# Optimization experiments

Measured on AMD Instinct MI355X. Metric: run time of the kernel, lower is better.

Reference implementation:

```python
import jax, jax.numpy as jnp
import numpy as np

N_ENT, N_REL, E, S, W, C = 1000000, 1000, 128, 8, 64, 1024


def setup_inputs() -> dict:
    key = jax.random.key(0)
    ks = jax.random.split(key, 12)
    sc = 0.02
    return {
        "ent_emb": jax.random.normal(ks[0], (N_ENT, E), jnp.float32),
        "rel_emb": jax.random.normal(ks[1], (N_REL, E), jnp.float32),
        "relation": jax.random.normal(ks[2], (E,), jnp.float32),
        "W1": jax.random.normal(ks[3], (3 * E, 3 * E), jnp.float32) * sc,
        "b1": jnp.zeros((3 * E,), jnp.float32),
        "W2": jax.random.normal(ks[4], (3 * E, 2 * E), jnp.float32) * sc,
        "b2": jnp.zeros((2 * E,), jnp.float32),
        "lstm_k": jax.random.normal(ks[5], (2 * E, 4 * E), jnp.float32) * sc,
        "lstm_r": jax.random.normal(ks[6], (E, 4 * E), jnp.float32) * sc,
        "lstm_b": jnp.zeros((4 * E,), jnp.float32),
        "cand_rel_ids": jax.random.randint(ks[7], (S, W, C), 0, N_REL),
        "cand_ent_ids": jax.random.randint(ks[8], (S, W, C), 0, N_ENT),
        "start_ent": jax.random.randint(ks[9], (W,), 0, N_ENT),
    }


def reference(ent_emb, rel_emb, relation, W1, b1, W2, b2, lstm_k, lstm_r, lstm_b,
              cand_rel_ids, cand_ent_ids, start_ent):
    # Batched, fixed-shape version of LSTMFinder.paths_between's hot loop:
    # per step: posterior MLP -> candidate gather+dot -> softmax -> global top-k
    # over (beam, candidate) -> LSTMCell state update for selected beams.
    rel_b = jnp.broadcast_to(relation, (W, E))

    def step(carry, xs):
        h, c, hist, cur = carry              # h,c,hist: [W,E]; cur: [W] int
        cr, ce = xs                          # [W,C] candidate rel/ent ids
        # posterior_mlp(concat(ent_enb, history_vector, relation))
        feat_in = jnp.concatenate([ent_emb[cur], hist, rel_b], axis=-1)   # [W,3E]
        hmid = jax.nn.relu(feat_in @ W1 + b1)
        feature = jax.nn.relu(hmid @ W2 + b2)                              # [W,2E]
        # candidate embeddings concat(rel_vec, ent_vec)
        cand_emb = jnp.concatenate([rel_emb[cr], ent_emb[ce]], axis=-1)    # [W,C,2E]
        scores = jnp.einsum('wcd,wd->wc', cand_emb, feature)               # [W,C]
        probs = jax.nn.softmax(scores, axis=-1)                            # per-path softmax
        # top_n_of_2d_choices over the full (beam, candidate) grid
        _, idx = jax.lax.top_k(probs.reshape(-1), W)
        parent = idx // C
        sel = idx % C
        inp = cand_emb[parent, sel]                                        # [W,2E]
        hp, cp = h[parent], c[parent]
        # keras LSTMCell: z = x@K + h@R + b, gates order i,f,g,o
        z = inp @ lstm_k + hp @ lstm_r + lstm_b
        i, f, g, o = jnp.split(z, 4, axis=-1)
        c_new = jax.nn.sigmoid(f) * cp + jax.nn.sigmoid(i) * jnp.tanh(g)
        h_new = jax.nn.sigmoid(o) * jnp.tanh(c_new)
        cur_new = ce[parent, sel]
        return (h_new, c_new, h_new, cur_new), probs

    z0 = jnp.zeros((W, E), jnp.float32)
    carry0 = (z0, z0, z0, start_ent)
    _, probs_all = jax.lax.scan(step, carry0, (cand_rel_ids, cand_ent_ids))
    return probs_all   # [S, W, C]
```

## Files before the change

kernel.cpp:

```cpp
#include <hip/hip_runtime.h>
#include <stdint.h>

#define E 128
#define W 64
#define C 1024
#define S 8
#define NBUCK 4096

typedef unsigned long long u64;
typedef unsigned int u32;

__device__ __forceinline__ float sigm(float x) { return 1.0f / (1.0f + expf(-x)); }

__device__ __forceinline__ int suffix_threshold(u32* hist, u32* wtot, int* s_B,
                                                int t, int lane, int wid) {
  const int b0 = t << 2;
  const u32 v0 = hist[b0], v1 = hist[b0 + 1], v2 = hist[b0 + 2], v3 = hist[b0 + 3];
  const u32 s3 = v3, s2 = v2 + s3, s1 = v1 + s2, s0 = v0 + s1;
  u32 incl = s0;
#pragma unroll
  for (int off = 1; off < 64; off <<= 1) {
    const u32 n = __shfl_down(incl, off, 64);
    if (lane + off < 64) incl += n;
  }
  if (lane == 0) wtot[wid] = incl;
  __syncthreads();
  u32 wsuf = 0;
  for (int i = wid + 1; i < 16; ++i) wsuf += wtot[i];
  const u32 above = wsuf + (incl - s0);
  hist[b0]     = above + s0;
  hist[b0 + 1] = above + s1;
  hist[b0 + 2] = above + s2;
  hist[b0 + 3] = above + s3;
  __syncthreads();
#pragma unroll
  for (int j = 0; j < 4; ++j) {
    const int b = b0 + j;
    const u32 here = hist[b];
    const u32 nxt = (b + 1 < NBUCK) ? hist[b + 1] : 0u;
    if (here >= 64u && nxt < 64u) *s_B = b;
  }
  __syncthreads();
  return *s_B;
}

__global__ __launch_bounds__(1024) void kA(
    int step,
    const float* __restrict__ ent_emb, const float* __restrict__ rel_emb,
    const float* __restrict__ relation,
    const float* __restrict__ W1, const float* __restrict__ b1,
    const float* __restrict__ W2, const float* __restrict__ b2,
    const float* __restrict__ lstm_k, const float* __restrict__ lstm_r,
    const float* __restrict__ lstm_b,
    const int* __restrict__ cand_rel_ids, const int* __restrict__ cand_ent_ids,
    const int* __restrict__ start_ent,
    float* __restrict__ Hst, float* __restrict__ Cst,
    float* __restrict__ rconstb,
    const u64* __restrict__ rowtop,
    float* __restrict__ featb)
{
  const int w = blockIdx.x, t = threadIdx.x;
  const int lane = t & 63, wid = t >> 6;
  __shared__ __align__(16) float xin[384];
  __shared__ __align__(16) float xcat2[256];
  __shared__ __align__(16) float z[512];
  __shared__ __align__(16) float hmid[384];
  __shared__ float sredpad[16];
  __shared__ u32 wtot[16];
  __shared__ int s_par, s_rid, s_eid, s_cnt, s_B;
  __shared__ __align__(16) unsigned char arena[32768];
  u32* hist = (u32*)arena;
  u64* coll = (u64*)arena;
  float4* zacc = (float4*)arena;
  (void)sredpad;

  float* Hn = Hst + (size_t)(step & 1) * W * E;
  float* Cn = Cst + (size_t)(step & 1) * W * E;
  const float* Hp = Hst + (size_t)((step + 1) & 1) * W * E;
  const float* Cp = Cst + (size_t)((step + 1) & 1) * W * E;

  if (step == 0) {
    const int cur = start_ent[w];
    if (t < 128) {
      xcat2[t] = ent_emb[(size_t)cur * E + t];
      xcat2[128 + t] = 0.f;
      Hn[w * E + t] = 0.f;
      Cn[w * E + t] = 0.f;
    }
    if (t < 384) {
      const int jg = t % 96, ks = t / 96;
      const int j0 = jg << 2, k0 = ks << 5;
      float4 acc = make_float4(0.f, 0.f, 0.f, 0.f);
#pragma unroll 8
      for (int kk = 0; kk < 32; ++kk) {
        const int k = k0 + kk;
        const float4 wt = *(const float4*)(W1 + (size_t)(256 + k) * 384 + j0);
        const float xk = relation[k];
        acc.x += xk * wt.x; acc.y += xk * wt.y;
        acc.z += xk * wt.z; acc.w += xk * wt.w;
      }
      zacc[t] = acc;
    }
    __syncthreads();
    if (t < 96) {
      float4 a = zacc[t];
#pragma unroll
      for (int sl = 1; sl < 4; ++sl) {
        const float4 bq = zacc[sl * 96 + t];
        a.x += bq.x; a.y += bq.y; a.z += bq.z; a.w += bq.w;
      }
      ((float4*)z)[t] = a;
      *(float4*)(rconstb + (t << 2)) = a;
    }
    __syncthreads();
  } else {
    if (t == 0) s_cnt = 0;
    ((uint4*)hist)[t] = make_uint4(0u, 0u, 0u, 0u);
    __syncthreads();
    u64 myk[4];
#pragma unroll
    for (int j = 0; j < 4; ++j) {
      myk[j] = rowtop[t + (j << 10)];
      atomicAdd(&hist[(u32)(myk[j] >> 51) & 0xFFFu], 1u);
    }
    __syncthreads();
    const int B = suffix_threshold(hist, wtot, &s_B, t, lane, wid);
#pragma unroll
    for (int j = 0; j < 4; ++j)
      if ((int)((myk[j] >> 51) & 0xFFFull) >= B) coll[atomicAdd(&s_cnt, 1)] = myk[j];
    __syncthreads();
    const int M = s_cnt;
    for (int i = t; i < M; i += 1024) {
      const u64 ki = coll[i];
      int r = 0;
      for (int j = 0; j < M; ++j) r += (coll[j] > ki);
      if (r == w) {
        const u32 flat = ~(u32)(ki & 0xFFFFFFFFull);
        const int p = (int)(flat >> 10);
        const int sl = (int)(flat & 1023u);
        const size_t cbase = (size_t)(step - 1) * W * C + (size_t)p * C + sl;
        s_par = p;
        s_rid = cand_rel_ids[cbase];
        s_eid = cand_ent_ids[cbase];
      }
    }
    __syncthreads();
    const int par = s_par, rid = s_rid, eid = s_eid;
    if (t < 384) {
      float v;
      if (t < 128) v = rel_emb[(size_t)rid * E + t];
      else if (t < 256) v = ent_emb[(size_t)eid * E + (t - 128)];
      else v = Hp[(size_t)par * E + (t - 256)];
      xin[t] = v;
    } else if (t < 512) {
      xcat2[t - 384] = ent_emb[(size_t)eid * E + (t - 384)];
    }
    __syncthreads();
    {
      const int ks = t >> 7, jg = t & 127;
      const int j0 = jg << 2, k0 = ks * 48;
      float4 acc = make_float4(0.f, 0.f, 0.f, 0.f);
#pragma unroll 8
      for (int kk = 0; kk < 48; ++kk) {
        const int k = k0 + kk;
        const float* Wp = (k < 256) ? (lstm_k + (size_t)k * 512 + j0)
                                    : (lstm_r + (size_t)(k - 256) * 512 + j0);
        const float4 wt = *(const float4*)Wp;
        const float xk = xin[k];
        acc.x += xk * wt.x; acc.y += xk * wt.y;
        acc.z += xk * wt.z; acc.w += xk * wt.w;
      }
      zacc[t] = acc;
    }
    __syncthreads();
    if (t < 128) {
      float4 a = zacc[t];
#pragma unroll
      for (int sl = 1; sl < 8; ++sl) {
        const float4 bq = zacc[sl * 128 + t];
        a.x += bq.x; a.y += bq.y; a.z += bq.z; a.w += bq.w;
      }
      const float4 bb = *(const float4*)(lstm_b + (t << 2));
      a.x += bb.x; a.y += bb.y; a.z += bb.z; a.w += bb.w;
      ((float4*)z)[t] = a;
    }
    __syncthreads();
    if (t < 128) {
      const float zi = z[t], zf = z[128 + t], zg = z[256 + t], zo = z[384 + t];
      const float cp = Cp[(size_t)par * E + t];
      const float cn = sigm(zf) * cp + sigm(zi) * tanhf(zg);
      const float hn = sigm(zo) * tanhf(cn);
      xcat2[128 + t] = hn;
      Hn[w * E + t] = hn;
      Cn[w * E + t] = cn;
    }
    __syncthreads();
  }

  if (t < 768) {
    const int jg = t % 96, ks = t / 96;
    const int j0 = jg << 2, k0 = ks << 5;
    float4 acc = make_float4(0.f, 0.f, 0.f, 0.f);
#pragma unroll 8
    for (int kk = 0; kk < 32; ++kk) {
      const int k = k0 + kk;
      const float4 wt = *(const float4*)(W1 + (size_t)k * 384 + j0);
      const float xk = xcat2[k];
      acc.x += xk * wt.x; acc.y += xk * wt.y;
      acc.z += xk * wt.z; acc.w += xk * wt.w;
    }
    zacc[t] = acc;
  }
  __syncthreads();
  if (t < 96) {
    float4 a = zacc[t];
#pragma unroll
    for (int sl = 1; sl < 8; ++sl) {
      const float4 bq = zacc[sl * 96 + t];
      a.x += bq.x; a.y += bq.y; a.z += bq.z; a.w += bq.w;
    }
    const float4 rc = (step == 0) ? ((const float4*)z)[t]
                                  : *(const float4*)(rconstb + (t << 2));
    const float4 bb = *(const float4*)(b1 + (t << 2));
    float4 hv;
    hv.x = fmaxf(a.x + rc.x + bb.x, 0.f);
    hv.y = fmaxf(a.y + rc.y + bb.y, 0.f);
    hv.z = fmaxf(a.z + rc.z + bb.z, 0.f);
    hv.w = fmaxf(a.w + rc.w + bb.w, 0.f);
    ((float4*)hmid)[t] = hv;
  }
  __syncthreads();

  {
    const int jg = t & 63, ks = t >> 6;
    const int j0 = jg << 2, k0 = ks * 24;
    float4 acc = make_float4(0.f, 0.f, 0.f, 0.f);
#pragma unroll 8
    for (int kk = 0; kk < 24; ++kk) {
      const int k = k0 + kk;
      const float4 wt = *(const float4*)(W2 + (size_t)k * 256 + j0);
      const float xk = hmid[k];
      acc.x += xk * wt.x; acc.y += xk * wt.y;
      acc.z += xk * wt.z; acc.w += xk * wt.w;
    }
    zacc[t] = acc;
  }
  __syncthreads();
  if (t < 64) {
    float4 a = zacc[t];
#pragma unroll
    for (int sl = 1; sl < 16; ++sl) {
      const float4 bq = zacc[sl * 64 + t];
      a.x += bq.x; a.y += bq.y; a.z += bq.z; a.w += bq.w;
    }
    const float4 bb = *(const float4*)(b2 + (t << 2));
    float4 fv;
    fv.x = fmaxf(a.x + bb.x, 0.f);
    fv.y = fmaxf(a.y + bb.y, 0.f);
    fv.z = fmaxf(a.z + bb.z, 0.f);
    fv.w = fmaxf(a.w + bb.w, 0.f);
    ((float4*)(featb + (size_t)w * 256))[t] = fv;
  }
}

__global__ __launch_bounds__(512) void kB(
    int step,
    const float* __restrict__ ent_emb, const float* __restrict__ rel_emb,
    const int* __restrict__ cand_rel_ids, const int* __restrict__ cand_ent_ids,
    const float* __restrict__ featb, float* __restrict__ scoresb)
{
  const int b = blockIdx.x, tid = threadIdx.x;
  const int w = b >> 3, c0 = (b & 7) << 7;
  __shared__ __align__(16) float featl[256];
  __shared__ int srid[128], seid[128];

  const size_t idbase = (size_t)step * W * C + (size_t)w * C + c0;
  if (tid < 256) featl[tid] = featb[(size_t)w * 256 + tid];
  else if (tid < 384) srid[tid - 256] = cand_rel_ids[idbase + (tid - 256)];
  else seid[tid - 384] = cand_ent_ids[idbase + (tid - 384)];
  __syncthreads();

  const int cl = tid >> 2, j = tid & 3;
  const float4* rp = (const float4*)(rel_emb + (size_t)srid[cl] * E);
  const float4* ep = (const float4*)(ent_emb + (size_t)seid[cl] * E);
  const float4* f4 = (const float4*)featl;
  float ax = 0.f, ay = 0.f, az = 0.f, aw = 0.f;
#pragma unroll
  for (int i = 0; i < 8; ++i) {
    const float4 r = rp[j + 4 * i], f = f4[j + 4 * i];
    ax += r.x * f.x; ay += r.y * f.y; az += r.z * f.z; aw += r.w * f.w;
  }
#pragma unroll
  for (int i = 0; i < 8; ++i) {
    const float4 e = ep[j + 4 * i], f = f4[32 + j + 4 * i];
    ax += e.x * f.x; ay += e.y * f.y; az += e.z * f.z; aw += e.w * f.w;
  }
  float acc = (ax + ay) + (az + aw);
  acc += __shfl_xor(acc, 1, 64);
  acc += __shfl_xor(acc, 2, 64);
  if (j == 0) scoresb[(size_t)w * C + c0 + cl] = acc;
}

__global__ __launch_bounds__(1024) void kC(
    int step, int last, const float* __restrict__ scoresb,
    float* __restrict__ out, u64* __restrict__ rowtop)
{
  const int w = blockIdx.x, t = threadIdx.x;
  const int lane = t & 63, wid = t >> 6;
  __shared__ float sred[16];
  __shared__ float s_m, s_inv;
  __shared__ u32 wtot[16];
  __shared__ int s_cnt, s_B;
  __shared__ __align__(16) unsigned char arena[32768];
  u32* hist = (u32*)arena;
  u64* coll = (u64*)arena;

  const float score = scoresb[(size_t)w * C + t];

  float v = score;
#pragma unroll
  for (int d = 32; d; d >>= 1) v = fmaxf(v, __shfl_xor(v, d, 64));
  if (lane == 0) sred[wid] = v;
  __syncthreads();
  if (t == 0) {
    float mm = sred[0];
#pragma unroll
    for (int i = 1; i < 16; ++i) mm = fmaxf(mm, sred[i]);
    s_m = mm;
  }
  __syncthreads();
  const float pexp = expf(score - s_m);
  v = pexp;
#pragma unroll
  for (int d = 32; d; d >>= 1) v += __shfl_xor(v, d, 64);
  if (lane == 0) sred[wid] = v;
  __syncthreads();
  if (t == 0) {
    float ss = sred[0];
#pragma unroll
    for (int i = 1; i < 16; ++i) ss += sred[i];
    s_inv = 1.f / ss;
  }
  __syncthreads();
  const float prob = pexp * s_inv;
  out[(size_t)step * W * C + (size_t)w * C + t] = prob;

  if (!last) {
    ((uint4*)hist)[t] = make_uint4(0u, 0u, 0u, 0u);
    if (t == 0) s_cnt = 0;
    __syncthreads();
    const u32 mono = __float_as_uint(prob) | 0x80000000u;
    const u64 key = ((u64)mono << 32) | (u32)~(u32)(w * C + t);
    atomicAdd(&hist[(mono >> 19) & 0xFFFu], 1u);
    __syncthreads();
    const int B = suffix_threshold(hist, wtot, &s_B, t, lane, wid);
    if ((int)((mono >> 19) & 0xFFFu) >= B) coll[atomicAdd(&s_cnt, 1)] = key;
    __syncthreads();
    const int M = s_cnt;
    for (int i = t; i < M; i += 1024) {
      const u64 ki = coll[i];
      int r = 0;
      for (int j = 0; j < M; ++j) r += (coll[j] > ki);
      if (r < 64) rowtop[(size_t)w * 64 + r] = ki;
    }
  }
}

extern "C" void kernel_launch(void* const* d_in, const int* in_sizes, int n_in,
                              void* d_out, int out_size, void* d_ws, size_t ws_size,
                              hipStream_t stream) {
  const float* ent_emb  = (const float*)d_in[0];
  const float* rel_emb  = (const float*)d_in[1];
  const float* relation = (const float*)d_in[2];
  const float* W1 = (const float*)d_in[3];
  const float* b1 = (const float*)d_in[4];
  const float* W2 = (const float*)d_in[5];
  const float* b2 = (const float*)d_in[6];
  const float* lstm_k = (const float*)d_in[7];
  const float* lstm_r = (const float*)d_in[8];
  const float* lstm_b = (const float*)d_in[9];
  const int* cr = (const int*)d_in[10];
  const int* ce = (const int*)d_in[11];
  const int* start_ent = (const int*)d_in[12];
  float* out = (float*)d_out;

  u64* rowtop = (u64*)d_ws;
  float* Hst = (float*)(rowtop + (size_t)W * 64);
  float* Cst = Hst + (size_t)2 * W * E;
  float* rconstb = Cst + (size_t)2 * W * E;
  float* featb = rconstb + 384;
  float* scoresb = featb + (size_t)W * 256;

  for (int s = 0; s < S; ++s) {
    kA<<<W, 1024, 0, stream>>>(s, ent_emb, rel_emb, relation, W1, b1, W2, b2,
                               lstm_k, lstm_r, lstm_b, cr, ce, start_ent,
                               Hst, Cst, rconstb, rowtop, featb);
    kB<<<512, 512, 0, stream>>>(s, ent_emb, rel_emb, cr, ce, featb, scoresb);
    kC<<<W, 1024, 0, stream>>>(s, (s == S - 1) ? 1 : 0, scoresb, out, rowtop);
  }
}
```

Baseline: 282.6 us.

## Move second MLP layer into scoring kernel split over four feature quarters

```diff
diff --git a/kernel.cpp b/kernel.cpp
--- a/kernel.cpp
+++ b/kernel.cpp
@@ -49,7 +49,6 @@
     const float* __restrict__ ent_emb, const float* __restrict__ rel_emb,
     const float* __restrict__ relation,
     const float* __restrict__ W1, const float* __restrict__ b1,
-    const float* __restrict__ W2, const float* __restrict__ b2,
     const float* __restrict__ lstm_k, const float* __restrict__ lstm_r,
     const float* __restrict__ lstm_b,
     const int* __restrict__ cand_rel_ids, const int* __restrict__ cand_ent_ids,
@@ -57,22 +56,19 @@
     float* __restrict__ Hst, float* __restrict__ Cst,
     float* __restrict__ rconstb,
     const u64* __restrict__ rowtop,
-    float* __restrict__ featb)
+    float* __restrict__ hmidb)
 {
   const int w = blockIdx.x, t = threadIdx.x;
   const int lane = t & 63, wid = t >> 6;
   __shared__ __align__(16) float xin[384];
   __shared__ __align__(16) float xcat2[256];
   __shared__ __align__(16) float z[512];
-  __shared__ __align__(16) float hmid[384];
-  __shared__ float sredpad[16];
   __shared__ u32 wtot[16];
   __shared__ int s_par, s_rid, s_eid, s_cnt, s_B;
   __shared__ __align__(16) unsigned char arena[32768];
   u32* hist = (u32*)arena;
   u64* coll = (u64*)arena;
   float4* zacc = (float4*)arena;
-  (void)sredpad;
 
   float* Hn = Hst + (size_t)(step & 1) * W * E;
   float* Cn = Cst + (size_t)(step & 1) * W * E;
@@ -227,82 +223,70 @@
     hv.y = fmaxf(a.y + rc.y + bb.y, 0.f);
     hv.z = fmaxf(a.z + rc.z + bb.z, 0.f);
     hv.w = fmaxf(a.w + rc.w + bb.w, 0.f);
-    ((float4*)hmid)[t] = hv;
-  }
-  __syncthreads();
-
-  {
-    const int jg = t & 63, ks = t >> 6;
-    const int j0 = jg << 2, k0 = ks * 24;
-    float4 acc = make_float4(0.f, 0.f, 0.f, 0.f);
-#pragma unroll 8
-    for (int kk = 0; kk < 24; ++kk) {
-      const int k = k0 + kk;
-      const float4 wt = *(const float4*)(W2 + (size_t)k * 256 + j0);
-      const float xk = hmid[k];
-      acc.x += xk * wt.x; acc.y += xk * wt.y;
-      acc.z += xk * wt.z; acc.w += xk * wt.w;
-    }
-    zacc[t] = acc;
-  }
-  __syncthreads();
-  if (t < 64) {
-    float4 a = zacc[t];
-#pragma unroll
-    for (int sl = 1; sl < 16; ++sl) {
-      const float4 bq = zacc[sl * 64 + t];
-      a.x += bq.x; a.y += bq.y; a.z += bq.z; a.w += bq.w;
-    }
-    const float4 bb = *(const float4*)(b2 + (t << 2));
-    float4 fv;
-    fv.x = fmaxf(a.x + bb.x, 0.f);
-    fv.y = fmaxf(a.y + bb.y, 0.f);
-    fv.z = fmaxf(a.z + bb.z, 0.f);
-    fv.w = fmaxf(a.w + bb.w, 0.f);
-    ((float4*)(featb + (size_t)w * 256))[t] = fv;
-  }
-}
-
-__global__ __launch_bounds__(512) void kB(
+    *(float4*)(hmidb + (size_t)w * 384 + (t << 2)) = hv;
+  }
+}
+
+__global__ __launch_bounds__(1024) void kB(
     int step,
     const float* __restrict__ ent_emb, const float* __restrict__ rel_emb,
+    const float* __restrict__ W2, const float* __restrict__ b2,
     const int* __restrict__ cand_rel_ids, const int* __restrict__ cand_ent_ids,
-    const float* __restrict__ featb, float* __restrict__ scoresb)
+    const float* __restrict__ hmidb, float* __restrict__ scores4)
 {
-  const int b = blockIdx.x, tid = threadIdx.x;
-  const int w = b >> 3, c0 = (b & 7) << 7;
-  __shared__ __align__(16) float featl[256];
-  __shared__ int srid[128], seid[128];
-
-  const size_t idbase = (size_t)step * W * C + (size_t)w * C + c0;
-  if (tid < 256) featl[tid] = featb[(size_t)w * 256 + tid];
-  else if (tid < 384) srid[tid - 256] = cand_rel_ids[idbase + (tid - 256)];
-  else seid[tid - 384] = cand_ent_ids[idbase + (tid - 384)];
-  __syncthreads();
-
-  const int cl = tid >> 2, j = tid & 3;
-  const float4* rp = (const float4*)(rel_emb + (size_t)srid[cl] * E);
-  const float4* ep = (const float4*)(ent_emb + (size_t)seid[cl] * E);
-  const float4* f4 = (const float4*)featl;
-  float ax = 0.f, ay = 0.f, az = 0.f, aw = 0.f;
-#pragma unroll
-  for (int i = 0; i < 8; ++i) {
-    const float4 r = rp[j + 4 * i], f = f4[j + 4 * i];
-    ax += r.x * f.x; ay += r.y * f.y; az += r.z * f.z; aw += r.w * f.w;
-  }
-#pragma unroll
-  for (int i = 0; i < 8; ++i) {
-    const float4 e = ep[j + 4 * i], f = f4[32 + j + 4 * i];
-    ax += e.x * f.x; ay += e.y * f.y; az += e.z * f.z; aw += e.w * f.w;
-  }
-  float acc = (ax + ay) + (az + aw);
-  acc += __shfl_xor(acc, 1, 64);
-  acc += __shfl_xor(acc, 2, 64);
-  if (j == 0) scoresb[(size_t)w * C + c0 + cl] = acc;
+  const int b = blockIdx.x, t = threadIdx.x;
+  const int w = b >> 2, q = b & 3;
+  __shared__ __align__(16) float hmidl[384];
+  __shared__ __align__(16) float zred[1024];
+  __shared__ __align__(16) float feats[64];
+
+  const size_t sbase = (size_t)step * W * C + (size_t)w * C + t;
+  const int rid = cand_rel_ids[sbase];
+  const int eid = cand_ent_ids[sbase];
+
+  if (t < 384) hmidl[t] = hmidb[(size_t)w * 384 + t];
+  __syncthreads();
+
+  {
+    const int o = t & 63, ks = t >> 6;
+    const int col = (q << 6) + o, k0 = ks * 24;
+    float a0 = 0.f, a1 = 0.f, a2 = 0.f, a3 = 0.f;
+#pragma unroll 6
+    for (int kk = 0; kk < 24; kk += 4) {
+      const int k = k0 + kk;
+      a0 += hmidl[k]     * W2[(size_t)(k)     * 256 + col];
+      a1 += hmidl[k + 1] * W2[(size_t)(k + 1) * 256 + col];
+      a2 += hmidl[k + 2] * W2[(size_t)(k + 2) * 256 + col];
+      a3 += hmidl[k + 3] * W2[(size_t)(k + 3) * 256 + col];
+    }
+    zred[t] = (a0 + a1) + (a2 + a3);
+  }
+  __syncthreads();
+  if (t < 64) {
+    float a = 0.f;
+#pragma unroll
+    for (int sl = 0; sl < 16; ++sl) a += zred[(sl << 6) + t];
+    feats[t] = fmaxf(a + b2[(q << 6) + t], 0.f);
+  }
+  __syncthreads();
+
+  {
+    const float4* row = (q < 2)
+        ? (const float4*)(rel_emb + (size_t)rid * E + (q << 6))
+        : (const float4*)(ent_emb + (size_t)eid * E + ((q - 2) << 6));
+    const float4* f4 = (const float4*)feats;
+    float ax = 0.f, ay = 0.f, az = 0.f, aw = 0.f;
+#pragma unroll
+    for (int i = 0; i < 16; ++i) {
+      const float4 r = row[i], f = f4[i];
+      ax += r.x * f.x; ay += r.y * f.y; az += r.z * f.z; aw += r.w * f.w;
+    }
+    scores4[((size_t)q * W + w) * C + t] = (ax + ay) + (az + aw);
+  }
 }
 
 __global__ __launch_bounds__(1024) void kC(
-    int step, int last, const float* __restrict__ scoresb,
+    int step, int last, const float* __restrict__ scores4,
     float* __restrict__ out, u64* __restrict__ rowtop)
 {
   const int w = blockIdx.x, t = threadIdx.x;
@@ -315,7 +299,11 @@
   u32* hist = (u32*)arena;
   u64* coll = (u64*)arena;
 
-  const float score = scoresb[(size_t)w * C + t];
+  const float p0 = scores4[((size_t)0 * W + w) * C + t];
+  const float p1 = scores4[((size_t)1 * W + w) * C + t];
+  const float p2 = scores4[((size_t)2 * W + w) * C + t];
+  const float p3 = scores4[((size_t)3 * W + w) * C + t];
+  const float score = (p0 + p1) + (p2 + p3);
 
   float v = score;
 #pragma unroll
@@ -388,14 +376,15 @@
   float* Hst = (float*)(rowtop + (size_t)W * 64);
   float* Cst = Hst + (size_t)2 * W * E;
   float* rconstb = Cst + (size_t)2 * W * E;
-  float* featb = rconstb + 384;
-  float* scoresb = featb + (size_t)W * 256;
+  float* hmidb = rconstb + 384;
+  float* scores4 = hmidb + (size_t)W * 384;
 
   for (int s = 0; s < S; ++s) {
-    kA<<<W, 1024, 0, stream>>>(s, ent_emb, rel_emb, relation, W1, b1, W2, b2,
+    kA<<<W, 1024, 0, stream>>>(s, ent_emb, rel_emb, relation, W1, b1,
                                lstm_k, lstm_r, lstm_b, cr, ce, start_ent,
-                               Hst, Cst, rconstb, rowtop, featb);
-    kB<<<512, 512, 0, stream>>>(s, ent_emb, rel_emb, cr, ce, featb, scoresb);
-    kC<<<W, 1024, 0, stream>>>(s, (s == S - 1) ? 1 : 0, scoresb, out, rowtop);
-  }
-}
+                               Hst, Cst, rconstb, rowtop, hmidb);
+    kB<<<W * 4, 1024, 0, stream>>>(s, ent_emb, rel_emb, W2, b2, cr, ce,
+                                   hmidb, scores4);
+    kC<<<W, 1024, 0, stream>>>(s, (s == S - 1) ? 1 : 0, scores4, out, rowtop);
+  }
+}
```

After: 334.9 us. 1.19x slower.

## Precompute relation-LSTM projections and skip zero ReLU rows in W2 matvec

Applied to the files above, without the earlier changes.

```diff
diff --git a/kernel.cpp b/kernel.cpp
--- a/kernel.cpp
+++ b/kernel.cpp
@@ -44,6 +44,36 @@
   return *s_B;
 }
 
+__global__ __launch_bounds__(1024) void kRelz(
+    const float* __restrict__ rel_emb, const float* __restrict__ lstm_k,
+    float* __restrict__ relz)
+{
+  const int b = blockIdx.x, t = threadIdx.x;
+  const int j = t & 511, h = t >> 9;
+  __shared__ float rl[4][128];
+  __shared__ float zr[1024];
+  const int r0 = b << 2;
+  for (int i = t; i < 4 * 128; i += 1024)
+    rl[i >> 7][i & 127] = rel_emb[(size_t)(r0 + (i >> 7)) * E + (i & 127)];
+  __syncthreads();
+  for (int rr = 0; rr < 4; ++rr) {
+    const int k0 = h << 6;
+    float a0 = 0.f, a1 = 0.f, a2 = 0.f, a3 = 0.f;
+#pragma unroll 4
+    for (int kk = 0; kk < 64; kk += 4) {
+      const int k = k0 + kk;
+      a0 += rl[rr][k]     * lstm_k[(size_t)(k)     * 512 + j];
+      a1 += rl[rr][k + 1] * lstm_k[(size_t)(k + 1) * 512 + j];
+      a2 += rl[rr][k + 2] * lstm_k[(size_t)(k + 2) * 512 + j];
+      a3 += rl[rr][k + 3] * lstm_k[(size_t)(k + 3) * 512 + j];
+    }
+    zr[t] = (a0 + a1) + (a2 + a3);
+    __syncthreads();
+    if (h == 0) relz[(size_t)(r0 + rr) * 512 + j] = zr[j] + zr[512 + j];
+    __syncthreads();
+  }
+}
+
 __global__ __launch_bounds__(1024) void kA(
     int step,
     const float* __restrict__ ent_emb, const float* __restrict__ rel_emb,
@@ -51,7 +81,7 @@
     const float* __restrict__ W1, const float* __restrict__ b1,
     const float* __restrict__ W2, const float* __restrict__ b2,
     const float* __restrict__ lstm_k, const float* __restrict__ lstm_r,
-    const float* __restrict__ lstm_b,
+    const float* __restrict__ lstm_b, const float* __restrict__ relz,
     const int* __restrict__ cand_rel_ids, const int* __restrict__ cand_ent_ids,
     const int* __restrict__ start_ent,
     float* __restrict__ Hst, float* __restrict__ Cst,
@@ -65,20 +95,21 @@
   __shared__ __align__(16) float xcat2[256];
   __shared__ __align__(16) float z[512];
   __shared__ __align__(16) float hmid[384];
-  __shared__ float sredpad[16];
   __shared__ u32 wtot[16];
   __shared__ int s_par, s_rid, s_eid, s_cnt, s_B;
+  __shared__ int nzidx[384];
+  __shared__ int woff[7];
   __shared__ __align__(16) unsigned char arena[32768];
   u32* hist = (u32*)arena;
   u64* coll = (u64*)arena;
   float4* zacc = (float4*)arena;
-  (void)sredpad;
 
   float* Hn = Hst + (size_t)(step & 1) * W * E;
   float* Cn = Cst + (size_t)(step & 1) * W * E;
   const float* Hp = Hst + (size_t)((step + 1) & 1) * W * E;
   const float* Cp = Cst + (size_t)((step + 1) & 1) * W * E;
 
+  int rid_sel = 0;
   if (step == 0) {
     const int cur = start_ent[w];
     if (t < 128) {
@@ -146,22 +177,22 @@
     }
     __syncthreads();
     const int par = s_par, rid = s_rid, eid = s_eid;
-    if (t < 384) {
+    rid_sel = rid;
+    if (t >= 128 && t < 384) {
       float v;
-      if (t < 128) v = rel_emb[(size_t)rid * E + t];
-      else if (t < 256) v = ent_emb[(size_t)eid * E + (t - 128)];
+      if (t < 256) v = ent_emb[(size_t)eid * E + (t - 128)];
       else v = Hp[(size_t)par * E + (t - 256)];
       xin[t] = v;
-    } else if (t < 512) {
+    } else if (t >= 384 && t < 512) {
       xcat2[t - 384] = ent_emb[(size_t)eid * E + (t - 384)];
     }
     __syncthreads();
     {
       const int ks = t >> 7, jg = t & 127;
-      const int j0 = jg << 2, k0 = ks * 48;
+      const int j0 = jg << 2, k0 = 128 + (ks << 5);
       float4 acc = make_float4(0.f, 0.f, 0.f, 0.f);
 #pragma unroll 8
-      for (int kk = 0; kk < 48; ++kk) {
+      for (int kk = 0; kk < 32; ++kk) {
         const int k = k0 + kk;
         const float* Wp = (k < 256) ? (lstm_k + (size_t)k * 512 + j0)
                                     : (lstm_r + (size_t)(k - 256) * 512 + j0);
@@ -180,8 +211,10 @@
         const float4 bq = zacc[sl * 128 + t];
         a.x += bq.x; a.y += bq.y; a.z += bq.z; a.w += bq.w;
       }
+      const float4 rz = *(const float4*)(relz + (size_t)rid * 512 + (t << 2));
       const float4 bb = *(const float4*)(lstm_b + (t << 2));
-      a.x += bb.x; a.y += bb.y; a.z += bb.z; a.w += bb.w;
+      a.x += rz.x + bb.x; a.y += rz.y + bb.y;
+      a.z += rz.z + bb.z; a.w += rz.w + bb.w;
       ((float4*)z)[t] = a;
     }
     __syncthreads();
@@ -196,6 +229,7 @@
     }
     __syncthreads();
   }
+  (void)rid_sel;
 
   if (t < 768) {
     const int jg = t % 96, ks = t / 96;
@@ -231,13 +265,33 @@
   }
   __syncthreads();
 
+  if (t < 384) {
+    const u64 mask = __ballot(hmid[t] > 0.f);
+    if ((t & 63) == 0) woff[(t >> 6) + 1] = __popcll(mask);
+  }
+  __syncthreads();
+  if (t == 0) {
+    woff[0] = 0;
+    for (int i = 1; i < 7; ++i) woff[i] += woff[i - 1];
+  }
+  __syncthreads();
+  if (t < 384) {
+    const u64 mask = __ballot(hmid[t] > 0.f);
+    if (hmid[t] > 0.f) {
+      const int pos = woff[t >> 6] +
+                      (int)__popcll(mask & ((1ull << (t & 63)) - 1ull));
+      nzidx[pos] = t;
+    }
+  }
+  __syncthreads();
+  const int nz = woff[6];
+
   {
     const int jg = t & 63, ks = t >> 6;
-    const int j0 = jg << 2, k0 = ks * 24;
+    const int j0 = jg << 2;
     float4 acc = make_float4(0.f, 0.f, 0.f, 0.f);
-#pragma unroll 8
-    for (int kk = 0; kk < 24; ++kk) {
-      const int k = k0 + kk;
+    for (int i = ks; i < nz; i += 16) {
+      const int k = nzidx[i];
       const float4 wt = *(const float4*)(W2 + (size_t)k * 256 + j0);
       const float xk = hmid[k];
       acc.x += xk * wt.x; acc.y += xk * wt.y;
@@ -390,10 +444,12 @@
   float* rconstb = Cst + (size_t)2 * W * E;
   float* featb = rconstb + 384;
   float* scoresb = featb + (size_t)W * 256;
-
+  float* relz = scoresb + (size_t)W * C;
+
+  kRelz<<<250, 1024, 0, stream>>>(rel_emb, lstm_k, relz);
   for (int s = 0; s < S; ++s) {
     kA<<<W, 1024, 0, stream>>>(s, ent_emb, rel_emb, relation, W1, b1, W2, b2,
-                               lstm_k, lstm_r, lstm_b, cr, ce, start_ent,
+                               lstm_k, lstm_r, lstm_b, relz, cr, ce, start_ent,
                                Hst, Cst, rconstb, rowtop, featb);
     kB<<<512, 512, 0, stream>>>(s, ent_emb, rel_emb, cr, ce, featb, scoresb);
     kC<<<W, 1024, 0, stream>>>(s, (s == S - 1) ? 1 : 0, scoresb, out, rowtop);
```

Measured after the change: 286.0 us. No clear change (+1.2%).
